# Optimization experiments

Measured on AMD Instinct MI355X. Metric: run time of the kernel, lower is better.

## Reference

```python
import jax, jax.numpy as jnp
import numpy as np

# Surrogate-gradient Heaviside spike (original repo uses @jax.custom_vjp spike_fn;
# forward is a hard step, backward uses a fast-sigmoid surrogate scaled by alpha).
@jax.custom_vjp
def spike_fn(x, alpha):
    return jnp.where(x > 0, 1.0, 0.0).astype(x.dtype)

def _spike_fwd(x, alpha):
    return spike_fn(x, alpha), (x, alpha)

def _spike_bwd(res, g):
    x, alpha = res
    surr = 1.0 / (alpha * jnp.abs(x) + 1.0) ** 2  # fast-sigmoid surrogate
    return (g * surr, jnp.zeros_like(alpha))

spike_fn.defvjp(_spike_fwd, _spike_bwd)


def setup_inputs() -> dict:
    key = jax.random.key(0)
    k1, k2 = jax.random.split(key)
    B, T, H, W, F = 8, 64, 16, 16, 256
    x = jax.random.normal(k1, (B, T, H, W, F), dtype=jnp.float32)
    w_rec = jax.random.normal(k2, (F, F), dtype=jnp.float32) * 0.05  # normal(stddev=0.05) init
    return {
        "x": x,
        "w_rec": w_rec,
        "hp_alif_d": jnp.float32(0.7),
        "hp_alif_adp": jnp.float32(0.9),
        "hp_alif_beta": jnp.float32(1.8),
        "hp_alpha": jnp.float32(2.0),
    }


def reference(x, w_rec, hp_alif_d, hp_alif_adp, hp_alif_beta, hp_alpha):
    # x: (B, T, H, W, F) -> time-major (T, B, H, W, F)
    x_seq = jnp.moveaxis(x, 1, 0)

    def scan_fn(carry, x_t):
        v, theta, prev_s = carry
        theta_next = theta * hp_alif_adp + prev_s * hp_alif_beta
        rec_input = jnp.dot(prev_s, w_rec)  # contract last (feature) dim
        v_next = v * hp_alif_d + x_t + rec_input
        vth_t = 0.5 + theta_next
        s = spike_fn(v_next - vth_t, hp_alpha)
        v_next = v_next - jax.lax.stop_gradient(s) * vth_t
        return (v_next, theta_next, s), s

    z = jnp.zeros_like(x_seq[0])
    _, spikes = jax.lax.scan(scan_fn, (z, z, z), x_seq)
    return jnp.moveaxis(spikes, 0, 1)  # back to (B, T, H, W, F)
```

## Files before the change

kernel.cpp:

```cpp
#include <hip/hip_runtime.h>


#define FDIM 256
#define TSTEPS 64
#define HWDIM 256

__global__ __launch_bounds__(256, 8) void alif_kernel(
    const float* __restrict__ x,
    const float* __restrict__ w_rec,
    const float* __restrict__ hp_d_p,
    const float* __restrict__ hp_adp_p,
    const float* __restrict__ hp_beta_p,
    float* __restrict__ out)
{
    const int tid  = threadIdx.x;
    const int blk  = blockIdx.x;
    const int wave = tid >> 6;
    const int lane = tid & 63;

    const float d    = hp_d_p[0];
    const float adp  = hp_adp_p[0];
    const float beta = hp_beta_p[0];

    __shared__ __align__(16) int list[FDIM];
    __shared__ __align__(16) int cnt[4];

    const int b  = blk >> 8;
    const int hw = blk & 255;
    size_t idx = (size_t)b * TSTEPS * (HWDIM * FDIM) + (size_t)hw * FDIM + tid;
    const size_t tstride = (size_t)HWDIM * FDIM;

    const int fbyte = tid << 2;
    const char* wb = (const char*)w_rec;

    float v = 0.f, th = 0.f, s = 0.f;

    for (int t = 0; t < TSTEPS; ++t) {
        float xt = x[idx];

        unsigned long long m = __ballot(s != 0.f);
        if (lane == 0) cnt[wave] = __popcll(m);
        __syncthreads();
        int4 c4 = *(const int4*)cnt;
        int base  = (wave > 0 ? c4.x : 0) + (wave > 1 ? c4.y : 0)
                  + (wave > 2 ? c4.z : 0);
        int total = c4.x + c4.y + c4.z + c4.w;
        if (s != 0.f) {
            int pos = base + __popcll(m & ((1ull << lane) - 1ull));
            list[pos] = tid << 10;
        }
        __syncthreads();

        float rec = 0.f;
        int i = 0;
        for (; i + 4 <= total; i += 4) {
            int4 ko = *(const int4*)&list[i];
            float w0 = *(const float*)(wb + (ko.x + fbyte));
            float w1 = *(const float*)(wb + (ko.y + fbyte));
            float w2 = *(const float*)(wb + (ko.z + fbyte));
            float w3 = *(const float*)(wb + (ko.w + fbyte));
            rec += w0; rec += w1; rec += w2; rec += w3;
        }
        for (; i < total; ++i) {
            int ko = list[i];
            rec += *(const float*)(wb + (ko + fbyte));
        }

        th = fmaf(th, adp, s * beta);
        float vn  = fmaf(v, d, xt) + rec;
        float vth = 0.5f + th;
        float sn  = (vn - vth) > 0.f ? 1.f : 0.f;
        v = vn - sn * vth;
        s = sn;
        out[idx] = sn;

        idx += tstride;
    }
}

extern "C" void kernel_launch(void* const* d_in, const int* in_sizes, int n_in,
                              void* d_out, int out_size, void* d_ws, size_t ws_size,
                              hipStream_t stream) {
    const float* x       = (const float*)d_in[0];
    const float* w_rec   = (const float*)d_in[1];
    const float* hp_d    = (const float*)d_in[2];
    const float* hp_adp  = (const float*)d_in[3];
    const float* hp_beta = (const float*)d_in[4];
    float* out = (float*)d_out;

    alif_kernel<<<2048, 256, 0, stream>>>(x, w_rec, hp_d, hp_adp, hp_beta, out);
}
```

Baseline: 395.3 us.

## Map one spatial site per wave with float4 features to drop block barriers

Each wavefront now owns a whole (b,hw) site and each lane handles four features as a float4. The spike list comes from four wave-uniform ballot masks walked with scalar bit tricks, so the shared-memory compaction and both __syncthreads per timestep go away. Weight rows are gathered as float4 in batches of eight with masking, and the next timestep's x is prefetched. The cost is a 4x smaller grid (512 blocks), more registers per thread, and wasted masked loads when the spike count is not a multiple of eight.

```diff
diff --git a/kernel.cpp b/kernel.cpp
--- a/kernel.cpp
+++ b/kernel.cpp
@@ -1,11 +1,15 @@
 #include <hip/hip_runtime.h>
 
 
-#define FDIM 256
 #define TSTEPS 64
-#define HWDIM 256
 
-__global__ __launch_bounds__(256, 8) void alif_kernel(
+__device__ __forceinline__ unsigned long long uniform_mask(unsigned long long m) {
+    unsigned lo = __builtin_amdgcn_readfirstlane((unsigned)m);
+    unsigned hi = __builtin_amdgcn_readfirstlane((unsigned)(m >> 32));
+    return (((unsigned long long)hi) << 32) | lo;
+}
+
+__global__ __launch_bounds__(256) void alif_kernel(
     const float* __restrict__ x,
     const float* __restrict__ w_rec,
     const float* __restrict__ hp_d_p,
@@ -13,68 +17,123 @@
     const float* __restrict__ hp_beta_p,
     float* __restrict__ out)
 {
-    const int tid  = threadIdx.x;
-    const int blk  = blockIdx.x;
-    const int wave = tid >> 6;
-    const int lane = tid & 63;
+    const int lane = threadIdx.x & 63;
+    const int wave = threadIdx.x >> 6;
+    const int site = (int)(blockIdx.x << 2) | wave;
+    const int b  = site >> 8;
+    const int hw = site & 255;
 
     const float d    = hp_d_p[0];
     const float adp  = hp_adp_p[0];
     const float beta = hp_beta_p[0];
 
-    __shared__ __align__(16) int list[FDIM];
-    __shared__ __align__(16) int cnt[4];
+    size_t xidx = (size_t)b * ((size_t)TSTEPS * 65536) + (size_t)hw * 256
+                + ((size_t)lane << 2);
+    const char* wb = (const char*)w_rec;
+    const int fb16 = lane << 4;
 
-    const int b  = blk >> 8;
-    const int hw = blk & 255;
-    size_t idx = (size_t)b * TSTEPS * (HWDIM * FDIM) + (size_t)hw * FDIM + tid;
-    const size_t tstride = (size_t)HWDIM * FDIM;
-
-    const int fbyte = tid << 2;
-    const char* wb = (const char*)w_rec;
-
-    float v = 0.f, th = 0.f, s = 0.f;
+    float4 v  = make_float4(0.f, 0.f, 0.f, 0.f);
+    float4 th = make_float4(0.f, 0.f, 0.f, 0.f);
+    float4 s  = make_float4(0.f, 0.f, 0.f, 0.f);
+    float4 xt = *(const float4*)(x + xidx);
 
     for (int t = 0; t < TSTEPS; ++t) {
-        float xt = x[idx];
+        unsigned long long m0 = uniform_mask(__ballot(s.x != 0.f));
+        unsigned long long m1 = uniform_mask(__ballot(s.y != 0.f));
+        unsigned long long m2 = uniform_mask(__ballot(s.z != 0.f));
+        unsigned long long m3 = uniform_mask(__ballot(s.w != 0.f));
+        unsigned long long any = m0 | m1 | m2 | m3;
 
-        unsigned long long m = __ballot(s != 0.f);
-        if (lane == 0) cnt[wave] = __popcll(m);
-        __syncthreads();
-        int4 c4 = *(const int4*)cnt;
-        int base  = (wave > 0 ? c4.x : 0) + (wave > 1 ? c4.y : 0)
-                  + (wave > 2 ? c4.z : 0);
-        int total = c4.x + c4.y + c4.z + c4.w;
-        if (s != 0.f) {
-            int pos = base + __popcll(m & ((1ull << lane) - 1ull));
-            list[pos] = tid << 10;
-        }
-        __syncthreads();
+        size_t nidx = xidx + (t < TSTEPS - 1 ? (size_t)65536 : (size_t)0);
+        float4 xn = *(const float4*)(x + nidx);
 
-        float rec = 0.f;
-        int i = 0;
-        for (; i + 4 <= total; i += 4) {
-            int4 ko = *(const int4*)&list[i];
-            float w0 = *(const float*)(wb + (ko.x + fbyte));
-            float w1 = *(const float*)(wb + (ko.y + fbyte));
-            float w2 = *(const float*)(wb + (ko.z + fbyte));
-            float w3 = *(const float*)(wb + (ko.w + fbyte));
-            rec += w0; rec += w1; rec += w2; rec += w3;
-        }
-        for (; i < total; ++i) {
-            int ko = list[i];
-            rec += *(const float*)(wb + (ko + fbyte));
+        float4 rec = make_float4(0.f, 0.f, 0.f, 0.f);
+
+        int l = 0; unsigned nib = 0u;
+        auto next = [&]() -> int {
+            while (nib == 0u) {
+                if (any == 0ull) return -1;
+                l = (int)__builtin_ctzll(any); any &= any - 1ull;
+                nib = (unsigned)(((m0 >> l) & 1ull)
+                               | (((m1 >> l) & 1ull) << 1)
+                               | (((m2 >> l) & 1ull) << 2)
+                               | (((m3 >> l) & 1ull) << 3));
+            }
+            int j = __builtin_ctz(nib); nib &= nib - 1u;
+            return (l << 2) + j;
+        };
+
+        int r0 = next();
+        while (r0 >= 0) {
+            int r1 = next(), r2 = next(), r3 = next();
+            int r4 = next(), r5 = next(), r6 = next(), r7 = next();
+            int a1 = r1 < 0 ? 0 : r1, a2 = r2 < 0 ? 0 : r2, a3 = r3 < 0 ? 0 : r3;
+            int a4 = r4 < 0 ? 0 : r4, a5 = r5 < 0 ? 0 : r5, a6 = r6 < 0 ? 0 : r6;
+            int a7 = r7 < 0 ? 0 : r7;
+            float4 w0 = *(const float4*)(wb + ((r0 << 10) + fb16));
+            float4 w1 = *(const float4*)(wb + ((a1 << 10) + fb16));
+            float4 w2 = *(const float4*)(wb + ((a2 << 10) + fb16));
+            float4 w3 = *(const float4*)(wb + ((a3 << 10) + fb16));
+            float4 w4 = *(const float4*)(wb + ((a4 << 10) + fb16));
+            float4 w5 = *(const float4*)(wb + ((a5 << 10) + fb16));
+            float4 w6 = *(const float4*)(wb + ((a6 << 10) + fb16));
+            float4 w7 = *(const float4*)(wb + ((a7 << 10) + fb16));
+            float mu1 = r1 >= 0 ? 1.f : 0.f, mu2 = r2 >= 0 ? 1.f : 0.f;
+            float mu3 = r3 >= 0 ? 1.f : 0.f, mu4 = r4 >= 0 ? 1.f : 0.f;
+            float mu5 = r5 >= 0 ? 1.f : 0.f, mu6 = r6 >= 0 ? 1.f : 0.f;
+            float mu7 = r7 >= 0 ? 1.f : 0.f;
+            rec.x += w0.x; rec.y += w0.y; rec.z += w0.z; rec.w += w0.w;
+            rec.x = fmaf(w1.x, mu1, rec.x); rec.y = fmaf(w1.y, mu1, rec.y);
+            rec.z = fmaf(w1.z, mu1, rec.z); rec.w = fmaf(w1.w, mu1, rec.w);
+            rec.x = fmaf(w2.x, mu2, rec.x); rec.y = fmaf(w2.y, mu2, rec.y);
+            rec.z = fmaf(w2.z, mu2, rec.z); rec.w = fmaf(w2.w, mu2, rec.w);
+            rec.x = fmaf(w3.x, mu3, rec.x); rec.y = fmaf(w3.y, mu3, rec.y);
+            rec.z = fmaf(w3.z, mu3, rec.z); rec.w = fmaf(w3.w, mu3, rec.w);
+            rec.x = fmaf(w4.x, mu4, rec.x); rec.y = fmaf(w4.y, mu4, rec.y);
+            rec.z = fmaf(w4.z, mu4, rec.z); rec.w = fmaf(w4.w, mu4, rec.w);
+            rec.x = fmaf(w5.x, mu5, rec.x); rec.y = fmaf(w5.y, mu5, rec.y);
+            rec.z = fmaf(w5.z, mu5, rec.z); rec.w = fmaf(w5.w, mu5, rec.w);
+            rec.x = fmaf(w6.x, mu6, rec.x); rec.y = fmaf(w6.y, mu6, rec.y);
+            rec.z = fmaf(w6.z, mu6, rec.z); rec.w = fmaf(w6.w, mu6, rec.w);
+            rec.x = fmaf(w7.x, mu7, rec.x); rec.y = fmaf(w7.y, mu7, rec.y);
+            rec.z = fmaf(w7.z, mu7, rec.z); rec.w = fmaf(w7.w, mu7, rec.w);
+            r0 = next();
         }
 
-        th = fmaf(th, adp, s * beta);
-        float vn  = fmaf(v, d, xt) + rec;
-        float vth = 0.5f + th;
-        float sn  = (vn - vth) > 0.f ? 1.f : 0.f;
-        v = vn - sn * vth;
+        float4 sn;
+        {
+            th.x = fmaf(th.x, adp, s.x * beta);
+            float vn = fmaf(v.x, d, xt.x) + rec.x;
+            float vt = 0.5f + th.x;
+            sn.x = (vn - vt) > 0.f ? 1.f : 0.f;
+            v.x = vn - sn.x * vt;
+        }
+        {
+            th.y = fmaf(th.y, adp, s.y * beta);
+            float vn = fmaf(v.y, d, xt.y) + rec.y;
+            float vt = 0.5f + th.y;
+            sn.y = (vn - vt) > 0.f ? 1.f : 0.f;
+            v.y = vn - sn.y * vt;
+        }
+        {
+            th.z = fmaf(th.z, adp, s.z * beta);
+            float vn = fmaf(v.z, d, xt.z) + rec.z;
+            float vt = 0.5f + th.z;
+            sn.z = (vn - vt) > 0.f ? 1.f : 0.f;
+            v.z = vn - sn.z * vt;
+        }
+        {
+            th.w = fmaf(th.w, adp, s.w * beta);
+            float vn = fmaf(v.w, d, xt.w) + rec.w;
+            float vt = 0.5f + th.w;
+            sn.w = (vn - vt) > 0.f ? 1.f : 0.f;
+            v.w = vn - sn.w * vt;
+        }
         s = sn;
-        out[idx] = sn;
+        *(float4*)(out + xidx) = s;
 
-        idx += tstride;
+        xidx = nidx;
+        xt = xn;
     }
 }
 
@@ -88,5 +147,5 @@
     const float* hp_beta = (const float*)d_in[4];
     float* out = (float*)d_out;
 
-    alif_kernel<<<2048, 256, 0, stream>>>(x, w_rec, hp_d, hp_adp, hp_beta, out);
+    alif_kernel<<<512, 256, 0, stream>>>(x, w_rec, hp_d, hp_adp, hp_beta, out);
 }
```

Result: slower. 445.4 us (+12.6%).
